# Kernel optimization log

Hardware: AMD Instinct MI355X
Metric: run time of the kernel (lower is better)

## Reference

```python
import jax, jax.numpy as jnp
import numpy as np

B, S, H = 2, 2048, 2048
N_HEADS = 16
HEAD_DIM = H // N_HEADS


def setup_inputs() -> dict:
    key = jax.random.key(0)
    ks = jax.random.split(key, 9)
    s = 1.0 / np.sqrt(H)
    inp = {
        "x": jax.random.normal(ks[0], (B, S, H), dtype=jnp.float32),
        "wq": jax.random.uniform(ks[1], (H, H), jnp.float32, -s, s),
        "bq": jnp.zeros((H,), jnp.float32),
        "wk": jax.random.uniform(ks[2], (H, H), jnp.float32, -s, s),
        "bk": jnp.zeros((H,), jnp.float32),
        "wv": jax.random.uniform(ks[3], (H, H), jnp.float32, -s, s),
        "bv": jnp.zeros((H,), jnp.float32),
        "wo": jax.random.uniform(ks[4], (H, H), jnp.float32, -s, s),
        "bo": jnp.zeros((H,), jnp.float32),
    }
    return inp


def reference(x, wq, bq, wk, bk, wv, bv, wo, bo):
    bsz, seq_len, hidden = x.shape
    scale = HEAD_DIM ** -0.5
    # projections -> [b, h, s, d]
    def proj(w, b):
        y = jnp.einsum("bsh,oh->bso", x, w) + b
        return y.reshape(bsz, seq_len, N_HEADS, HEAD_DIM).transpose(0, 2, 1, 3)
    q = proj(wq, bq)
    k = proj(wk, bk)
    v = proj(wv, bv)
    scores = jnp.einsum("bhqd,bhkd->bhqk", q, k) * scale
    causal = jnp.tril(jnp.ones((seq_len, seq_len), dtype=bool))
    scores = jnp.where(causal, scores, -jnp.inf)
    attn = jax.nn.softmax(scores, axis=-1)
    out = jnp.einsum("bhqk,bhkd->bhqd", attn, v)
    out = out.transpose(0, 2, 1, 3).reshape(bsz, seq_len, hidden)
    return jnp.einsum("bsh,oh->bso", out, wo) + bo
```

## Files before the change

kernel.cpp:

```cpp
#include <hip/hip_runtime.h>
#include <hip/hip_bf16.h>
#include <cstdint>
#include <cstddef>

#define BATCH 2
#define S_LEN 2048
#define HID   2048
#define NH    16
#define HD    128
#define GK    2048
#define NT    (GK / 64)
#define NIT   (NT / 2)
#define ATT_TILES (32 * NH * BATCH)

typedef short bf16x8 __attribute__((ext_vector_type(8)));
typedef float f32x4  __attribute__((ext_vector_type(4)));

__device__ inline unsigned short f2bf(float f) {
    unsigned int u = __float_as_uint(f);
    unsigned int r = (u + 0x7fffu + ((u >> 16) & 1u)) >> 16;
    return (unsigned short)r;
}

__global__ __launch_bounds__(256) void conv_f32_bf16(const float* __restrict__ src,
                                                     unsigned short* __restrict__ dst,
                                                     long n) {
    long i = ((long)blockIdx.x * 256 + threadIdx.x) * 8;
    if (i >= n) return;
    const float4 a = *(const float4*)(src + i);
    const float4 b = *(const float4*)(src + i + 4);
    union { unsigned short u[8]; bf16x8 v; } o;
    o.u[0] = f2bf(a.x); o.u[1] = f2bf(a.y); o.u[2] = f2bf(a.z); o.u[3] = f2bf(a.w);
    o.u[4] = f2bf(b.x); o.u[5] = f2bf(b.y); o.u[6] = f2bf(b.z); o.u[7] = f2bf(b.w);
    *(bf16x8*)(dst + i) = o.v;
}

__global__ __launch_bounds__(256) void conv4_f32_bf16(const float* __restrict__ s0,
                                                      const float* __restrict__ s1,
                                                      const float* __restrict__ s2,
                                                      const float* __restrict__ s3,
                                                      unsigned short* __restrict__ d0,
                                                      unsigned short* __restrict__ d1,
                                                      unsigned short* __restrict__ d2,
                                                      unsigned short* __restrict__ d3,
                                                      long n) {
    const int z = blockIdx.y;
    const float* src = (z == 0) ? s0 : (z == 1) ? s1 : (z == 2) ? s2 : s3;
    unsigned short* dst = (z == 0) ? d0 : (z == 1) ? d1 : (z == 2) ? d2 : d3;
    long i = ((long)blockIdx.x * 256 + threadIdx.x) * 8;
    if (i >= n) return;
    const float4 a = *(const float4*)(src + i);
    const float4 b = *(const float4*)(src + i + 4);
    union { unsigned short u[8]; bf16x8 v; } o;
    o.u[0] = f2bf(a.x); o.u[1] = f2bf(a.y); o.u[2] = f2bf(a.z); o.u[3] = f2bf(a.w);
    o.u[4] = f2bf(b.x); o.u[5] = f2bf(b.y); o.u[6] = f2bf(b.z); o.u[7] = f2bf(b.w);
    *(bf16x8*)(dst + i) = o.v;
}

__global__ void zero_int(int* p) { *p = 0; }


#define STAGE(DU, SRC, KT, H) do {                                            \
    const unsigned short* _s0 = (SRC) + (size_t)((H) * 128) * GK + (KT) * 64; \
    __builtin_amdgcn_global_load_lds(                                         \
        (const __attribute__((address_space(1))) void*)_s0,                   \
        (__attribute__((address_space(3))) void*)(Sm + (DU) + (H) * 8192 + sdst), \
        16, 0, 0);                                                            \
    __builtin_amdgcn_global_load_lds(                                         \
        (const __attribute__((address_space(1))) void*)(_s0 + (size_t)64 * GK), \
        (__attribute__((address_space(3))) void*)(Sm + (DU) + (H) * 8192 + 4096 + sdst), \
        16, 0, 0);                                                            \
} while (0)

#define READ_A(D, HI) do { _Pragma("unroll")                                  \
    for (int mi = 0; mi < 4; ++mi) {                                          \
        const int r_ = wm * 128 + (HI) * 64 + mi * 16 + ln;                   \
        a[mi][0] = *(const bf16x8*)&Sm[(D) * 32768 + r_ * 64 + sw0];          \
        a[mi][1] = *(const bf16x8*)&Sm[(D) * 32768 + r_ * 64 + sw1];          \
    } } while (0)

#define READ_B(D, SEL) do { _Pragma("unroll")                                 \
    for (int ni = 0; ni < 2; ++ni) {                                          \
        const int r_ = wn * 64 + ((SEL) * 2 + ni) * 16 + ln;                  \
        b[(SEL)*2+ni][0] = *(const bf16x8*)&Sm[(D) * 32768 + 16384 + r_ * 64 + sw0]; \
        b[(SEL)*2+ni][1] = *(const bf16x8*)&Sm[(D) * 32768 + 16384 + r_ * 64 + sw1]; \
    } } while (0)

#define MFMA16(MB, NS) do { _Pragma("unroll")                                 \
    for (int mi = 0; mi < 4; ++mi) _Pragma("unroll")                          \
    for (int ni = 0; ni < 2; ++ni) _Pragma("unroll")                          \
    for (int ks = 0; ks < 2; ++ks)                                            \
        acc[(MB)+mi][(NS)*2+ni] = __builtin_amdgcn_mfma_f32_16x16x32_bf16(    \
            a[mi][ks], b[(NS)*2+ni][ks], acc[(MB)+mi][(NS)*2+ni], 0, 0, 0);   \
} while (0)

#define PH_BEGIN  __builtin_amdgcn_s_barrier();                               \
                  asm volatile("s_waitcnt lgkmcnt(0)" ::: "memory");          \
                  __builtin_amdgcn_s_setprio(1)
#define PH_END    __builtin_amdgcn_s_setprio(0); __builtin_amdgcn_s_barrier()
#define PH_END_V4 __builtin_amdgcn_s_setprio(0);                              \
                  asm volatile("s_waitcnt vmcnt(4)" ::: "memory");            \
                  __builtin_amdgcn_s_barrier()

__device__ __forceinline__ void gemm256_core(const unsigned short* __restrict__ A,
                                             const unsigned short* __restrict__ Bw,
                                             const float* __restrict__ bias,
                                             void* __restrict__ Cout,
                                             int mode, int M0, int N0,
                                             unsigned short* Sm) {
    const int tid  = threadIdx.x;
    const int lane = tid & 63;
    const int wave = tid >> 6;
    const int ln = lane & 15, g = lane >> 4;
    const int wm = wave & 1, wn = wave >> 1;

    const int strow = tid >> 3;
    const int stcol = (((tid & 7) ^ ((tid >> 3) & 7)) << 3);
    const unsigned short* gA = A  + (size_t)(M0 + strow) * GK + stcol;
    const unsigned short* gB = Bw + (size_t)(N0 + strow) * GK + stcol;
    const int sdst = wave * 512;

    const int sw0 = ((g    ) ^ (ln & 7)) << 3;
    const int sw1 = ((g + 4) ^ (ln & 7)) << 3;

    f32x4 acc[8][4];
#pragma unroll
    for (int i = 0; i < 8; ++i)
#pragma unroll
        for (int j = 0; j < 4; ++j) acc[i][j] = (f32x4){0.f, 0.f, 0.f, 0.f};
    bf16x8 a[4][2], b[4][2];

    STAGE(0,     gA, 0, 0); STAGE(0,     gA, 0, 1);
    STAGE(16384, gB, 0, 0); STAGE(16384, gB, 0, 1);
    STAGE(32768, gA, 1, 0); STAGE(32768, gA, 1, 1);
    asm volatile("s_waitcnt vmcnt(4)" ::: "memory");
    __builtin_amdgcn_s_barrier();

    for (int it = 0; it < NIT; ++it) {
        const int kt1 = 2 * it + 1;
        const int kt2 = (2 * it + 2 < NT) ? 2 * it + 2 : NT - 1;
        const int kt3 = (2 * it + 3 < NT) ? 2 * it + 3 : NT - 1;
        READ_A(0, 0); READ_B(0, 0);
        STAGE(49152, gB, kt1, 0);
        PH_BEGIN; MFMA16(0, 0); PH_END;
        READ_B(0, 1);
        STAGE(49152, gB, kt1, 1);
        PH_BEGIN; MFMA16(0, 1); PH_END;
        READ_A(0, 1);
        STAGE(16384, gB, kt2, 0);
        PH_BEGIN; MFMA16(4, 0); PH_END;
        STAGE(16384, gB, kt2, 1);
        PH_BEGIN; MFMA16(4, 1); PH_END_V4;
        READ_A(1, 0); READ_B(1, 0);
        STAGE(0, gA, kt2, 0);
        PH_BEGIN; MFMA16(0, 0); PH_END;
        READ_B(1, 1);
        STAGE(0, gA, kt2, 1);
        PH_BEGIN; MFMA16(0, 1); PH_END;
        READ_A(1, 1);
        PH_BEGIN; MFMA16(4, 0); PH_END;
        STAGE(32768, gA, kt3, 0); STAGE(32768, gA, kt3, 1);
        PH_BEGIN; MFMA16(4, 1); PH_END_V4;
    }
    asm volatile("s_waitcnt vmcnt(0)" ::: "memory");
    __syncthreads();

    if (mode == 0) {
        const int bb = M0 >> 11;
        const int sb = M0 & (S_LEN - 1);
#pragma unroll
        for (int nf = 0; nf < 4; ++nf) {
            const int n = N0 + wn * 64 + nf * 16 + ln;
            const float bn = bias[n];
            const int h = n >> 7, d = n & (HD - 1);
            unsigned short* dst = (unsigned short*)Cout +
                (((size_t)(bb * NH + h) * S_LEN + sb + wm * 128) * HD + d);
#pragma unroll
            for (int mf = 0; mf < 8; ++mf)
#pragma unroll
                for (int r = 0; r < 4; ++r)
                    dst[(size_t)(mf * 16 + g * 4 + r) * HD] = f2bf(acc[mf][nf][r] + bn);
        }
    } else if (mode == 2) {
        float* dst = (float*)Cout;
#pragma unroll
        for (int nf = 0; nf < 4; ++nf) {
            const int n = N0 + wn * 64 + nf * 16 + ln;
            const float bn = bias[n];
#pragma unroll
            for (int mf = 0; mf < 8; ++mf)
#pragma unroll
                for (int r = 0; r < 4; ++r) {
                    const int m = M0 + wm * 128 + mf * 16 + g * 4 + r;
                    dst[(size_t)m * HID + n] = acc[mf][nf][r] + bn;
                }
        }
    } else {
        const int bb = M0 >> 11;
        const int sb = M0 & (S_LEN - 1);
#pragma unroll
        for (int p = 0; p < 2; ++p) {
            if ((wn >> 1) == p) {
#pragma unroll
                for (int nf = 0; nf < 4; ++nf) {
                    const int dl = (wn & 1) * 64 + nf * 16 + ln;
                    const float bn = bias[N0 + p * 128 + dl];
#pragma unroll
                    for (int mf = 0; mf < 8; ++mf) {
                        const int sl = wm * 128 + mf * 16 + g * 4;
                        const int cs = (sl >> 3) ^ (dl & 31);
                        union { unsigned short u[4]; unsigned long long q; } pk;
#pragma unroll
                        for (int r = 0; r < 4; ++r) pk.u[r] = f2bf(acc[mf][nf][r] + bn);
                        *(unsigned long long*)&Sm[dl * 256 + cs * 8 + (sl & 7)] = pk.q;
                    }
                }
            }
            __syncthreads();
            {
                const int dl = tid >> 2;
                const int h = (N0 >> 7) + p;
                unsigned short* dst = (unsigned short*)Cout +
                    ((size_t)(bb * NH + h) * HD + dl) * S_LEN + sb;
#pragma unroll
                for (int jj = 0; jj < 8; ++jj) {
                    const int sc = (tid & 3) + jj * 4;
                    const int cs = sc ^ (dl & 31);
                    *(bf16x8*)(dst + sc * 8) = *(const bf16x8*)&Sm[dl * 256 + cs * 8];
                }
            }
            __syncthreads();
        }
    }
}

__global__ __launch_bounds__(512, 2) void gemm_qkv256(
        const unsigned short* __restrict__ A,
        const unsigned short* __restrict__ w0, const unsigned short* __restrict__ w1,
        const unsigned short* __restrict__ w2,
        const float* __restrict__ b0, const float* __restrict__ b1,
        const float* __restrict__ b2,
        void* o0, void* o1, void* o2) {
    extern __shared__ __align__(16) unsigned short Sm[];
    const int z = blockIdx.z;
    const unsigned short* Bw = (z == 0) ? w0 : (z == 1) ? w1 : w2;
    const float* bias = (z == 0) ? b0 : (z == 1) ? b1 : b2;
    void* Cout = (z == 0) ? o0 : (z == 1) ? o1 : o2;
    gemm256_core(A, Bw, bias, Cout, (z == 2) ? 1 : 0,
                 blockIdx.y * 256, blockIdx.x * 256, Sm);
}

__global__ __launch_bounds__(512, 2) void gemm_out256(
        const unsigned short* __restrict__ A, const unsigned short* __restrict__ Bw,
        const float* __restrict__ bias, float* __restrict__ Cout) {
    extern __shared__ __align__(16) unsigned short Sm[];
    gemm256_core(A, Bw, bias, Cout, 2, blockIdx.y * 256, blockIdx.x * 256, Sm);
}

__global__ __launch_bounds__(256) void attn_kernel(const unsigned short* __restrict__ Q,
                                                   const unsigned short* __restrict__ Kk,
                                                   const unsigned short* __restrict__ Vt,
                                                   unsigned short* __restrict__ O,
                                                   int* __restrict__ ticket) {
    __shared__ __align__(16) unsigned short Ks[64 * 128];
    __shared__ __align__(16) unsigned short Vs[144 * 64];
    __shared__ __align__(16) unsigned short Pl[4][16 * 72];
    __shared__ int tsh;
    const int tid = threadIdx.x;
    const int lane = tid & 63;
    const int wave = tid >> 6;
    const int g = lane >> 4, ln = lane & 15;
    const float scale2 = 0.08838834764831845f * 1.4426950408889634f;

    for (int i = tid; i < 16 * 64; i += 256) Vs[128 * 64 + i] = 0x3F80;

    const int kcol = ((tid & 15) ^ ((tid >> 4) & 15)) * 8;
    const int vcol = ((tid & 7) ^ ((tid >> 3) & 7)) * 8;

    for (;;) {
        if (tid == 0) tsh = atomicAdd(ticket, 1);
        __syncthreads();
        const int t = tsh;
        if (t >= ATT_TILES) break;
        const int qt = 31 - (t >> 5);
        const int bh = t & 31;
        const int qbase = qt * 64 + wave * 16;

        const unsigned short* Qp = Q  + (size_t)bh * S_LEN * HD;
        const unsigned short* Kp = Kk + (size_t)bh * S_LEN * HD;
        const unsigned short* Vp = Vt + (size_t)bh * HD * S_LEN;

        bf16x8 aq[4];
#pragma unroll
        for (int dc = 0; dc < 4; ++dc)
            aq[dc] = *(const bf16x8*)&Qp[(size_t)(qbase + ln) * HD + dc * 32 + g * 8];

        f32x4 acc[9];
#pragma unroll
        for (int i = 0; i < 9; ++i) acc[i] = (f32x4){0.f, 0.f, 0.f, 0.f};

        for (int kt = 0; kt <= qt; ++kt) {
            const int kb = kt * 64;
#pragma unroll
            for (int i = 0; i < 4; ++i) {
                const unsigned short* gk = Kp + (size_t)(kb + i * 16 + (tid >> 4)) * HD + kcol;
                __builtin_amdgcn_global_load_lds(
                    (const __attribute__((address_space(1))) void*)gk,
                    (__attribute__((address_space(3))) void*)(Ks + i * 2048 + wave * 512),
                    16, 0, 0);
            }
#pragma unroll
            for (int i = 0; i < 4; ++i) {
                const unsigned short* gv = Vp + (size_t)(i * 32 + (tid >> 3)) * S_LEN + kb + vcol;
                __builtin_amdgcn_global_load_lds(
                    (const __attribute__((address_space(1))) void*)gv,
                    (__attribute__((address_space(3))) void*)(Vs + i * 2048 + wave * 512),
                    16, 0, 0);
            }
            __syncthreads();
            f32x4 sc[4];
#pragma unroll
            for (int nc = 0; nc < 4; ++nc) {
                sc[nc] = (f32x4){0.f, 0.f, 0.f, 0.f};
#pragma unroll
                for (int dc = 0; dc < 4; ++dc) {
                    bf16x8 bk = *(const bf16x8*)&Ks[(nc * 16 + ln) * 128 + ((dc * 4 + g) ^ ln) * 8];
                    sc[nc] = __builtin_amdgcn_mfma_f32_16x16x32_bf16(aq[dc], bk, sc[nc], 0, 0, 0);
                }
            }
            const bool diag = (kt == qt);
#pragma unroll
            for (int nc = 0; nc < 4; ++nc)
#pragma unroll
                for (int r = 0; r < 4; ++r) {
                    float pv = __builtin_amdgcn_exp2f(sc[nc][r] * scale2);
                    if (diag && (nc * 16 + ln > wave * 16 + g * 4 + r)) pv = 0.f;
                    Pl[wave][(g * 4 + r) * 72 + nc * 16 + ln] = f2bf(pv);
                }
#pragma unroll
            for (int kc = 0; kc < 2; ++kc) {
                bf16x8 ap = *(const bf16x8*)&Pl[wave][ln * 72 + kc * 32 + g * 8];
#pragma unroll
                for (int d2 = 0; d2 < 9; ++d2) {
                    bf16x8 bv = *(const bf16x8*)&Vs[(d2 * 16 + ln) * 64 + ((kc * 4 + g) ^ (ln & 7)) * 8];
                    acc[d2] = __builtin_amdgcn_mfma_f32_16x16x32_bf16(ap, bv, acc[d2], 0, 0, 0);
                }
            }
            __syncthreads();
        }
        const int b = bh >> 4, h = bh & 15;
        float inv[4];
#pragma unroll
        for (int r = 0; r < 4; ++r) inv[r] = 1.0f / acc[8][r];
#pragma unroll
        for (int d2 = 0; d2 < 8; ++d2)
#pragma unroll
            for (int r = 0; r < 4; ++r) {
                const int row = qbase + g * 4 + r;
                const int col = h * HD + d2 * 16 + ln;
                O[((size_t)b * S_LEN + row) * HID + col] = f2bf(acc[d2][r] * inv[r]);
            }
    }
}

extern "C" void kernel_launch(void* const* d_in, const int* in_sizes, int n_in,
                              void* d_out, int out_size, void* d_ws, size_t ws_size,
                              hipStream_t stream) {
    const float* x  = (const float*)d_in[0];
    const float* wq = (const float*)d_in[1];
    const float* bq = (const float*)d_in[2];
    const float* wk = (const float*)d_in[3];
    const float* bk = (const float*)d_in[4];
    const float* wv = (const float*)d_in[5];
    const float* bv = (const float*)d_in[6];
    const float* wo = (const float*)d_in[7];
    const float* bo = (const float*)d_in[8];
    float* out = (float*)d_out;

    const long nx = (long)BATCH * S_LEN * HID;
    const long nw = (long)HID * HID;

    char* p = (char*)d_ws;
    unsigned short* xb  = (unsigned short*)p; p += nx * 2;
    unsigned short* wqb = (unsigned short*)p; p += nw * 2;
    unsigned short* wkb = (unsigned short*)p; p += nw * 2;
    unsigned short* wvb = (unsigned short*)p; p += nw * 2;
    unsigned short* wob = (unsigned short*)p; p += nw * 2;
    unsigned short* Qb  = (unsigned short*)p; p += nx * 2;
    unsigned short* Kb  = (unsigned short*)p; p += nx * 2;
    unsigned short* Vtb = (unsigned short*)p; p += nx * 2;
    unsigned short* Ob  = (unsigned short*)p; p += nx * 2;
    int* ticket = (int*)p;

    conv_f32_bf16<<<(int)(nx / 8 / 256), 256, 0, stream>>>(x, xb, nx);
    dim3 cgrid((unsigned)(nw / 8 / 256), 4);
    conv4_f32_bf16<<<cgrid, 256, 0, stream>>>(wq, wk, wv, wo, wqb, wkb, wvb, wob, nw);
    zero_int<<<1, 1, 0, stream>>>(ticket);

    const int M = BATCH * S_LEN;
    dim3 qkvgrid(HID / 256, M / 256, 3);
    gemm_qkv256<<<qkvgrid, 512, 131072, stream>>>(xb, wqb, wkb, wvb, bq, bk, bv,
                                                  Qb, Kb, Vtb);

    attn_kernel<<<768, 256, 0, stream>>>(Qb, Kb, Vtb, Ob, ticket);

    dim3 ogrid(HID / 256, M / 256);
    gemm_out256<<<ogrid, 512, 131072, stream>>>(Ob, wob, bo, out);
}
```

Before: 400.7 us.

## Double-buffer K tiles in LDS and load V directly from global into registers

K tiles are now double-buffered in shared memory, and the next tile is prefetched while the current one is used, so one barrier per iteration is removed. V is no longer staged through LDS. Each wave reads its V fragments straight from global memory into registers, and the row-sum column comes from a constant ones vector instead of a padded LDS region. Launch bounds now request 3 blocks per CU. In exchange, every wave makes redundant global V loads that rely on cache hits, and register pressure goes up.

```diff
diff --git a/kernel.cpp b/kernel.cpp
--- a/kernel.cpp
+++ b/kernel.cpp
@@ -257,13 +257,12 @@
     gemm256_core(A, Bw, bias, Cout, 2, blockIdx.y * 256, blockIdx.x * 256, Sm);
 }
 
-__global__ __launch_bounds__(256) void attn_kernel(const unsigned short* __restrict__ Q,
-                                                   const unsigned short* __restrict__ Kk,
-                                                   const unsigned short* __restrict__ Vt,
-                                                   unsigned short* __restrict__ O,
-                                                   int* __restrict__ ticket) {
-    __shared__ __align__(16) unsigned short Ks[64 * 128];
-    __shared__ __align__(16) unsigned short Vs[144 * 64];
+__global__ __launch_bounds__(256, 3) void attn_kernel(const unsigned short* __restrict__ Q,
+                                                      const unsigned short* __restrict__ Kk,
+                                                      const unsigned short* __restrict__ Vt,
+                                                      unsigned short* __restrict__ O,
+                                                      int* __restrict__ ticket) {
+    __shared__ __align__(16) unsigned short Ks[2 * 64 * 128];
     __shared__ __align__(16) unsigned short Pl[4][16 * 72];
     __shared__ int tsh;
     const int tid = threadIdx.x;
@@ -271,11 +270,9 @@
     const int wave = tid >> 6;
     const int g = lane >> 4, ln = lane & 15;
     const float scale2 = 0.08838834764831845f * 1.4426950408889634f;
-
-    for (int i = tid; i < 16 * 64; i += 256) Vs[128 * 64 + i] = 0x3F80;
+    const bf16x8 ones_v = {0x3F80, 0x3F80, 0x3F80, 0x3F80, 0x3F80, 0x3F80, 0x3F80, 0x3F80};
 
     const int kcol = ((tid & 15) ^ ((tid >> 4) & 15)) * 8;
-    const int vcol = ((tid & 7) ^ ((tid >> 3) & 7)) * 8;
 
     for (;;) {
         if (tid == 0) tsh = atomicAdd(ticket, 1);
@@ -295,39 +292,50 @@
         for (int dc = 0; dc < 4; ++dc)
             aq[dc] = *(const bf16x8*)&Qp[(size_t)(qbase + ln) * HD + dc * 32 + g * 8];
 
+#pragma unroll
+        for (int i = 0; i < 4; ++i) {
+            const unsigned short* gk = Kp + (size_t)(i * 16 + (tid >> 4)) * HD + kcol;
+            __builtin_amdgcn_global_load_lds(
+                (const __attribute__((address_space(1))) void*)gk,
+                (__attribute__((address_space(3))) void*)(Ks + i * 2048 + wave * 512),
+                16, 0, 0);
+        }
+
         f32x4 acc[9];
 #pragma unroll
         for (int i = 0; i < 9; ++i) acc[i] = (f32x4){0.f, 0.f, 0.f, 0.f};
+
+        __syncthreads();
 
         for (int kt = 0; kt <= qt; ++kt) {
             const int kb = kt * 64;
-#pragma unroll
-            for (int i = 0; i < 4; ++i) {
-                const unsigned short* gk = Kp + (size_t)(kb + i * 16 + (tid >> 4)) * HD + kcol;
-                __builtin_amdgcn_global_load_lds(
-                    (const __attribute__((address_space(1))) void*)gk,
-                    (__attribute__((address_space(3))) void*)(Ks + i * 2048 + wave * 512),
-                    16, 0, 0);
-            }
-#pragma unroll
-            for (int i = 0; i < 4; ++i) {
-                const unsigned short* gv = Vp + (size_t)(i * 32 + (tid >> 3)) * S_LEN + kb + vcol;
-                __builtin_amdgcn_global_load_lds(
-                    (const __attribute__((address_space(1))) void*)gv,
-                    (__attribute__((address_space(3))) void*)(Vs + i * 2048 + wave * 512),
-                    16, 0, 0);
-            }
-            __syncthreads();
+            const int kbuf = (kt & 1) * 8192;
+            if (kt < qt) {
+                const int kb2 = kb + 64;
+                unsigned short* kdst = Ks + ((kt + 1) & 1) * 8192 + wave * 512;
+#pragma unroll
+                for (int i = 0; i < 4; ++i) {
+                    const unsigned short* gk = Kp + (size_t)(kb2 + i * 16 + (tid >> 4)) * HD + kcol;
+                    __builtin_amdgcn_global_load_lds(
+                        (const __attribute__((address_space(1))) void*)gk,
+                        (__attribute__((address_space(3))) void*)(kdst + i * 2048),
+                        16, 0, 0);
+                }
+            }
             f32x4 sc[4];
 #pragma unroll
             for (int nc = 0; nc < 4; ++nc) {
                 sc[nc] = (f32x4){0.f, 0.f, 0.f, 0.f};
 #pragma unroll
                 for (int dc = 0; dc < 4; ++dc) {
-                    bf16x8 bk = *(const bf16x8*)&Ks[(nc * 16 + ln) * 128 + ((dc * 4 + g) ^ ln) * 8];
+                    bf16x8 bk = *(const bf16x8*)&Ks[kbuf + (nc * 16 + ln) * 128 + ((dc * 4 + g) ^ ln) * 8];
                     sc[nc] = __builtin_amdgcn_mfma_f32_16x16x32_bf16(aq[dc], bk, sc[nc], 0, 0, 0);
                 }
             }
+            bf16x8 vv0[8], vv1[8];
+#pragma unroll
+            for (int d2 = 0; d2 < 8; ++d2)
+                vv0[d2] = *(const bf16x8*)&Vp[(size_t)(d2 * 16 + ln) * S_LEN + kb + g * 8];
             const bool diag = (kt == qt);
 #pragma unroll
             for (int nc = 0; nc < 4; ++nc)
@@ -338,13 +346,21 @@
                     Pl[wave][(g * 4 + r) * 72 + nc * 16 + ln] = f2bf(pv);
                 }
 #pragma unroll
-            for (int kc = 0; kc < 2; ++kc) {
-                bf16x8 ap = *(const bf16x8*)&Pl[wave][ln * 72 + kc * 32 + g * 8];
-#pragma unroll
-                for (int d2 = 0; d2 < 9; ++d2) {
-                    bf16x8 bv = *(const bf16x8*)&Vs[(d2 * 16 + ln) * 64 + ((kc * 4 + g) ^ (ln & 7)) * 8];
-                    acc[d2] = __builtin_amdgcn_mfma_f32_16x16x32_bf16(ap, bv, acc[d2], 0, 0, 0);
-                }
+            for (int d2 = 0; d2 < 8; ++d2)
+                vv1[d2] = *(const bf16x8*)&Vp[(size_t)(d2 * 16 + ln) * S_LEN + kb + (4 + g) * 8];
+            {
+                bf16x8 ap = *(const bf16x8*)&Pl[wave][ln * 72 + g * 8];
+#pragma unroll
+                for (int d2 = 0; d2 < 8; ++d2)
+                    acc[d2] = __builtin_amdgcn_mfma_f32_16x16x32_bf16(ap, vv0[d2], acc[d2], 0, 0, 0);
+                acc[8] = __builtin_amdgcn_mfma_f32_16x16x32_bf16(ap, ones_v, acc[8], 0, 0, 0);
+            }
+            {
+                bf16x8 ap = *(const bf16x8*)&Pl[wave][ln * 72 + 32 + g * 8];
+#pragma unroll
+                for (int d2 = 0; d2 < 8; ++d2)
+                    acc[d2] = __builtin_amdgcn_mfma_f32_16x16x32_bf16(ap, vv1[d2], acc[d2], 0, 0, 0);
+                acc[8] = __builtin_amdgcn_mfma_f32_16x16x32_bf16(ap, ones_v, acc[8], 0, 0, 0);
             }
             __syncthreads();
         }
```

After: 509.1 us. 1.27x slower.

## Shrink GEMM block tile from 256x256 to 256x128 with 4x2 wave layout

Applied to the files above, without the earlier changes.

Changes the QKV and output-projection GEMM tiles from 256x256 to 256x128 (M x N). The waves are rearranged 4x2, each computing a 64x64 sub-tile, and the LDS layout, staging schedule, wait counts and epilogues are rewritten to match. This doubles the number of blocks for better CU fill and cuts LDS use to 96KB. The cost is lower arithmetic intensity per block and more redundant A-tile loads.

```diff
diff --git a/kernel.cpp b/kernel.cpp
--- a/kernel.cpp
+++ b/kernel.cpp
@@ -73,31 +73,34 @@
 } while (0)
 
 #define READ_A(D, HI) do { _Pragma("unroll")                                  \
-    for (int mi = 0; mi < 4; ++mi) {                                          \
-        const int r_ = wm * 128 + (HI) * 64 + mi * 16 + ln;                   \
-        a[mi][0] = *(const bf16x8*)&Sm[(D) * 32768 + r_ * 64 + sw0];          \
-        a[mi][1] = *(const bf16x8*)&Sm[(D) * 32768 + r_ * 64 + sw1];          \
+    for (int mi = 0; mi < 2; ++mi) {                                          \
+        const int r_ = wm * 64 + ((HI) * 2 + mi) * 16 + ln;                   \
+        a[(HI)*2+mi][0] = *(const bf16x8*)&Sm[(D) * 24576 + r_ * 64 + sw0];   \
+        a[(HI)*2+mi][1] = *(const bf16x8*)&Sm[(D) * 24576 + r_ * 64 + sw1];   \
     } } while (0)
 
-#define READ_B(D, SEL) do { _Pragma("unroll")                                 \
+#define READ_B(D, HI) do { _Pragma("unroll")                                  \
     for (int ni = 0; ni < 2; ++ni) {                                          \
-        const int r_ = wn * 64 + ((SEL) * 2 + ni) * 16 + ln;                  \
-        b[(SEL)*2+ni][0] = *(const bf16x8*)&Sm[(D) * 32768 + 16384 + r_ * 64 + sw0]; \
-        b[(SEL)*2+ni][1] = *(const bf16x8*)&Sm[(D) * 32768 + 16384 + r_ * 64 + sw1]; \
+        const int r_ = wn * 64 + ((HI) * 2 + ni) * 16 + ln;                   \
+        b[(HI)*2+ni][0] = *(const bf16x8*)&Sm[(D) * 24576 + 16384 + r_ * 64 + sw0]; \
+        b[(HI)*2+ni][1] = *(const bf16x8*)&Sm[(D) * 24576 + 16384 + r_ * 64 + sw1]; \
     } } while (0)
 
-#define MFMA16(MB, NS) do { _Pragma("unroll")                                 \
-    for (int mi = 0; mi < 4; ++mi) _Pragma("unroll")                          \
+#define MFMA8(MA, NA) do { _Pragma("unroll")                                  \
+    for (int mi = 0; mi < 2; ++mi) _Pragma("unroll")                          \
     for (int ni = 0; ni < 2; ++ni) _Pragma("unroll")                          \
     for (int ks = 0; ks < 2; ++ks)                                            \
-        acc[(MB)+mi][(NS)*2+ni] = __builtin_amdgcn_mfma_f32_16x16x32_bf16(    \
-            a[mi][ks], b[(NS)*2+ni][ks], acc[(MB)+mi][(NS)*2+ni], 0, 0, 0);   \
+        acc[(MA)*2+mi][(NA)*2+ni] = __builtin_amdgcn_mfma_f32_16x16x32_bf16(  \
+            a[(MA)*2+mi][ks], b[(NA)*2+ni][ks], acc[(MA)*2+mi][(NA)*2+ni], 0, 0, 0); \
 } while (0)
 
 #define PH_BEGIN  __builtin_amdgcn_s_barrier();                               \
                   asm volatile("s_waitcnt lgkmcnt(0)" ::: "memory");          \
                   __builtin_amdgcn_s_setprio(1)
 #define PH_END    __builtin_amdgcn_s_setprio(0); __builtin_amdgcn_s_barrier()
+#define PH_END_V2 __builtin_amdgcn_s_setprio(0);                              \
+                  asm volatile("s_waitcnt vmcnt(2)" ::: "memory");            \
+                  __builtin_amdgcn_s_barrier()
 #define PH_END_V4 __builtin_amdgcn_s_setprio(0);                              \
                   asm volatile("s_waitcnt vmcnt(4)" ::: "memory");            \
                   __builtin_amdgcn_s_barrier()
@@ -112,7 +115,7 @@
     const int lane = tid & 63;
     const int wave = tid >> 6;
     const int ln = lane & 15, g = lane >> 4;
-    const int wm = wave & 1, wn = wave >> 1;
+    const int wm = wave & 3, wn = wave >> 2;
 
     const int strow = tid >> 3;
     const int stcol = (((tid & 7) ^ ((tid >> 3) & 7)) << 3);
@@ -123,16 +126,16 @@
     const int sw0 = ((g    ) ^ (ln & 7)) << 3;
     const int sw1 = ((g + 4) ^ (ln & 7)) << 3;
 
-    f32x4 acc[8][4];
-#pragma unroll
-    for (int i = 0; i < 8; ++i)
+    f32x4 acc[4][4];
+#pragma unroll
+    for (int i = 0; i < 4; ++i)
 #pragma unroll
         for (int j = 0; j < 4; ++j) acc[i][j] = (f32x4){0.f, 0.f, 0.f, 0.f};
     bf16x8 a[4][2], b[4][2];
 
     STAGE(0,     gA, 0, 0); STAGE(0,     gA, 0, 1);
-    STAGE(16384, gB, 0, 0); STAGE(16384, gB, 0, 1);
-    STAGE(32768, gA, 1, 0); STAGE(32768, gA, 1, 1);
+    STAGE(16384, gB, 0, 0);
+    STAGE(24576, gA, 1, 0); STAGE(24576, gA, 1, 1);
     asm volatile("s_waitcnt vmcnt(4)" ::: "memory");
     __builtin_amdgcn_s_barrier();
 
@@ -141,26 +144,24 @@
         const int kt2 = (2 * it + 2 < NT) ? 2 * it + 2 : NT - 1;
         const int kt3 = (2 * it + 3 < NT) ? 2 * it + 3 : NT - 1;
         READ_A(0, 0); READ_B(0, 0);
-        STAGE(49152, gB, kt1, 0);
-        PH_BEGIN; MFMA16(0, 0); PH_END;
+        STAGE(40960, gB, kt1, 0);
+        PH_BEGIN; MFMA8(0, 0); PH_END;
         READ_B(0, 1);
-        STAGE(49152, gB, kt1, 1);
-        PH_BEGIN; MFMA16(0, 1); PH_END;
+        PH_BEGIN; MFMA8(0, 1); PH_END;
         READ_A(0, 1);
         STAGE(16384, gB, kt2, 0);
-        PH_BEGIN; MFMA16(4, 0); PH_END;
-        STAGE(16384, gB, kt2, 1);
-        PH_BEGIN; MFMA16(4, 1); PH_END_V4;
+        PH_BEGIN; MFMA8(1, 0); PH_END;
+        PH_BEGIN; MFMA8(1, 1); PH_END_V2;
         READ_A(1, 0); READ_B(1, 0);
         STAGE(0, gA, kt2, 0);
-        PH_BEGIN; MFMA16(0, 0); PH_END;
+        PH_BEGIN; MFMA8(0, 0); PH_END;
         READ_B(1, 1);
         STAGE(0, gA, kt2, 1);
-        PH_BEGIN; MFMA16(0, 1); PH_END;
+        PH_BEGIN; MFMA8(0, 1); PH_END;
         READ_A(1, 1);
-        PH_BEGIN; MFMA16(4, 0); PH_END;
-        STAGE(32768, gA, kt3, 0); STAGE(32768, gA, kt3, 1);
-        PH_BEGIN; MFMA16(4, 1); PH_END_V4;
+        PH_BEGIN; MFMA8(1, 0); PH_END;
+        STAGE(24576, gA, kt3, 0); STAGE(24576, gA, kt3, 1);
+        PH_BEGIN; MFMA8(1, 1); PH_END_V4;
     }
     asm volatile("s_waitcnt vmcnt(0)" ::: "memory");
     __syncthreads();
@@ -168,15 +169,15 @@
     if (mode == 0) {
         const int bb = M0 >> 11;
         const int sb = M0 & (S_LEN - 1);
+        const int h  = N0 >> 7;
 #pragma unroll
         for (int nf = 0; nf < 4; ++nf) {
-            const int n = N0 + wn * 64 + nf * 16 + ln;
-            const float bn = bias[n];
-            const int h = n >> 7, d = n & (HD - 1);
+            const int d = wn * 64 + nf * 16 + ln;
+            const float bn = bias[N0 + d];
             unsigned short* dst = (unsigned short*)Cout +
-                (((size_t)(bb * NH + h) * S_LEN + sb + wm * 128) * HD + d);
-#pragma unroll
-            for (int mf = 0; mf < 8; ++mf)
+                (((size_t)(bb * NH + h) * S_LEN + sb + wm * 64) * HD + d);
+#pragma unroll
+            for (int mf = 0; mf < 4; ++mf)
 #pragma unroll
                 for (int r = 0; r < 4; ++r)
                     dst[(size_t)(mf * 16 + g * 4 + r) * HD] = f2bf(acc[mf][nf][r] + bn);
@@ -188,45 +189,45 @@
             const int n = N0 + wn * 64 + nf * 16 + ln;
             const float bn = bias[n];
 #pragma unroll
-            for (int mf = 0; mf < 8; ++mf)
+            for (int mf = 0; mf < 4; ++mf)
 #pragma unroll
                 for (int r = 0; r < 4; ++r) {
-                    const int m = M0 + wm * 128 + mf * 16 + g * 4 + r;
+                    const int m = M0 + wm * 64 + mf * 16 + g * 4 + r;
                     dst[(size_t)m * HID + n] = acc[mf][nf][r] + bn;
                 }
         }
     } else {
         const int bb = M0 >> 11;
         const int sb = M0 & (S_LEN - 1);
+        const int h  = N0 >> 7;
 #pragma unroll
         for (int p = 0; p < 2; ++p) {
-            if ((wn >> 1) == p) {
+            if ((wm >> 1) == p) {
 #pragma unroll
                 for (int nf = 0; nf < 4; ++nf) {
-                    const int dl = (wn & 1) * 64 + nf * 16 + ln;
-                    const float bn = bias[N0 + p * 128 + dl];
-#pragma unroll
-                    for (int mf = 0; mf < 8; ++mf) {
-                        const int sl = wm * 128 + mf * 16 + g * 4;
-                        const int cs = (sl >> 3) ^ (dl & 31);
+                    const int dl = wn * 64 + nf * 16 + ln;
+                    const float bn = bias[N0 + dl];
+#pragma unroll
+                    for (int mf = 0; mf < 4; ++mf) {
+                        const int sl = (wm & 1) * 64 + mf * 16 + g * 4;
+                        const int cs = (sl >> 3) ^ (dl & 15);
                         union { unsigned short u[4]; unsigned long long q; } pk;
 #pragma unroll
                         for (int r = 0; r < 4; ++r) pk.u[r] = f2bf(acc[mf][nf][r] + bn);
-                        *(unsigned long long*)&Sm[dl * 256 + cs * 8 + (sl & 7)] = pk.q;
+                        *(unsigned long long*)&Sm[dl * 128 + cs * 8 + (sl & 7)] = pk.q;
                     }
                 }
             }
             __syncthreads();
             {
                 const int dl = tid >> 2;
-                const int h = (N0 >> 7) + p;
                 unsigned short* dst = (unsigned short*)Cout +
-                    ((size_t)(bb * NH + h) * HD + dl) * S_LEN + sb;
-#pragma unroll
-                for (int jj = 0; jj < 8; ++jj) {
+                    ((size_t)(bb * NH + h) * HD + dl) * S_LEN + sb + p * 128;
+#pragma unroll
+                for (int jj = 0; jj < 4; ++jj) {
                     const int sc = (tid & 3) + jj * 4;
-                    const int cs = sc ^ (dl & 31);
-                    *(bf16x8*)(dst + sc * 8) = *(const bf16x8*)&Sm[dl * 256 + cs * 8];
+                    const int cs = sc ^ (dl & 15);
+                    *(bf16x8*)(dst + sc * 8) = *(const bf16x8*)&Sm[dl * 128 + cs * 8];
                 }
             }
             __syncthreads();
@@ -247,14 +248,14 @@
     const float* bias = (z == 0) ? b0 : (z == 1) ? b1 : b2;
     void* Cout = (z == 0) ? o0 : (z == 1) ? o1 : o2;
     gemm256_core(A, Bw, bias, Cout, (z == 2) ? 1 : 0,
-                 blockIdx.y * 256, blockIdx.x * 256, Sm);
+                 blockIdx.y * 256, blockIdx.x * 128, Sm);
 }
 
 __global__ __launch_bounds__(512, 2) void gemm_out256(
         const unsigned short* __restrict__ A, const unsigned short* __restrict__ Bw,
         const float* __restrict__ bias, float* __restrict__ Cout) {
     extern __shared__ __align__(16) unsigned short Sm[];
-    gemm256_core(A, Bw, bias, Cout, 2, blockIdx.y * 256, blockIdx.x * 256, Sm);
+    gemm256_core(A, Bw, bias, Cout, 2, blockIdx.y * 256, blockIdx.x * 128, Sm);
 }
 
 __global__ __launch_bounds__(256) void attn_kernel(const unsigned short* __restrict__ Q,
@@ -398,12 +399,12 @@
     zero_int<<<1, 1, 0, stream>>>(ticket);
 
     const int M = BATCH * S_LEN;
-    dim3 qkvgrid(HID / 256, M / 256, 3);
-    gemm_qkv256<<<qkvgrid, 512, 131072, stream>>>(xb, wqb, wkb, wvb, bq, bk, bv,
-                                                  Qb, Kb, Vtb);
+    dim3 qkvgrid(HID / 128, M / 256, 3);
+    gemm_qkv256<<<qkvgrid, 512, 98304, stream>>>(xb, wqb, wkb, wvb, bq, bk, bv,
+                                                 Qb, Kb, Vtb);
 
     attn_kernel<<<768, 256, 0, stream>>>(Qb, Kb, Vtb, Ob, ticket);
 
-    dim3 ogrid(HID / 256, M / 256);
-    gemm_out256<<<ogrid, 512, 131072, stream>>>(Ob, wob, bo, out);
-}
+    dim3 ogrid(HID / 128, M / 256);
+    gemm_out256<<<ogrid, 512, 98304, stream>>>(Ob, wob, bo, out);
+}
```

Result: faster. 374.5 us (-6.5%).
